# Optimization experiments

Measured on AMD Instinct MI355X. Metric: run time of the kernel, lower is better.

Reference implementation:

```python
import jax, jax.numpy as jnp
import numpy as np

B, N, C, OUT, E = 2, 512, 256, 256, 18


def setup_inputs() -> dict:
    key = jax.random.key(0)
    ks = jax.random.split(key, 16)
    s = 0.05
    w = lambda k, shape: jax.random.normal(k, shape, jnp.float32) * s
    return dict(
        x=jax.random.normal(ks[0], (B, N, C), jnp.float32),
        adjacency=jax.random.randint(ks[1], (B, N, N), 0, 2, jnp.int32),
        edge_feats=jax.random.normal(ks[2], (B, N, N, E), jnp.float32),
        st_w=w(ks[3], (C, OUT)), st_b=jnp.zeros((OUT,), jnp.float32),
        nt_w=w(ks[4], (C, OUT)), nt_b=jnp.zeros((OUT,), jnp.float32),
        em_w1=w(ks[5], (E, 64)), em_b1=jnp.zeros((64,), jnp.float32),
        em_w2=w(ks[6], (64, 64)), em_b2=jnp.zeros((64,), jnp.float32),
        em_w3=w(ks[7], (64, 32)), em_b3=jnp.zeros((32,), jnp.float32),
        at_w1=w(ks[8], (2 * C + 32, 64)), at_b1=jnp.zeros((64,), jnp.float32),
        at_w2=w(ks[9], (64, 32)), at_b2=jnp.zeros((32,), jnp.float32),
        at_w3=w(ks[10], (32, 1)), at_b3=jnp.zeros((1,), jnp.float32),
        eg_w1=w(ks[11], (C + 32, 64)), eg_b1=jnp.zeros((64,), jnp.float32),
        eg_w2=w(ks[12], (64, OUT)), eg_b2=jnp.zeros((OUT,), jnp.float32),
        cb_w1=w(ks[13], (2 * OUT, OUT)), cb_b1=jnp.zeros((OUT,), jnp.float32),
        cb_w2=w(ks[14], (OUT, OUT)), cb_b2=jnp.zeros((OUT,), jnp.float32),
    )


def reference(x, adjacency, edge_feats,
              st_w, st_b, nt_w, nt_b,
              em_w1, em_b1, em_w2, em_b2, em_w3, em_b3,
              at_w1, at_b1, at_w2, at_b2, at_w3, at_b3,
              eg_w1, eg_b1, eg_w2, eg_b2,
              cb_w1, cb_b1, cb_w2, cb_b2):
    c = x.shape[-1]
    mask = adjacency > 0                      # [B,N,N] neighbor mask (j axis = neighbors of i)
    maskf = mask.astype(x.dtype)
    self_feat = x @ st_w + st_b               # [B,N,OUT]
    nbr = x @ nt_w + nt_b                     # [B,N,OUT] transformed neighbor feats
    # edge MLP 18->64->64->32
    pe = jax.nn.relu(edge_feats @ em_w1 + em_b1)
    pe = jax.nn.relu(pe @ em_w2 + em_b2)
    pe = jax.nn.relu(pe @ em_w3 + em_b3)      # [B,N,N,32]
    # attention MLP on concat(x_i, x_j, pe): split first layer to avoid [B,N,N,2C+32]
    a_i = x @ at_w1[:c]                       # [B,N,64]
    a_j = x @ at_w1[c:2 * c]                  # [B,N,64]
    a_e = pe @ at_w1[2 * c:]                  # [B,N,N,64]
    h = jax.nn.relu(a_i[:, :, None, :] + a_j[:, None, :, :] + a_e + at_b1)
    h = jax.nn.relu(h @ at_w2 + at_b2)        # [B,N,N,32]
    scores = (h @ at_w3)[..., 0] + at_b3[0]   # [B,N,N]
    scores = jnp.where(mask, scores, jnp.asarray(-1e9, x.dtype))
    attn = jax.nn.softmax(scores, axis=-1) * maskf  # softmax over neighbor set of each i
    # edge gate on concat(x_j, pe): split first layer
    g = jax.nn.relu((x @ eg_w1[:c])[:, None, :, :] + pe @ eg_w1[c:] + eg_b1)
    g = jax.nn.sigmoid(g @ eg_w2 + eg_b2)     # [B,N,N,OUT]
    gated = g * nbr[:, None, :, :]            # [B,N,N,OUT]
    msg = jnp.einsum('bij,bijc->bic', attn, gated)
    has_nbr = mask.any(axis=-1)[..., None].astype(x.dtype)
    msg = msg * has_nbr                        # nodes with no neighbors get zero message
    comb = jnp.concatenate([self_feat, msg], axis=-1)
    out = jax.nn.relu(comb @ cb_w1 + cb_b1) @ cb_w2 + cb_b2
    return out
```

## Files before the change

### kernel.cpp

```cpp
#include <hip/hip_runtime.h>

#define BB 2
#define NN 512
#define CC 256
#define OO 256
#define EE 18

#define OFF_SF   0
#define OFF_NBR  (BB*NN*OO)
#define OFF_AI   (OFF_NBR + BB*NN*OO)
#define OFF_AJ   (OFF_AI + BB*NN*64)
#define OFF_EGX  (OFF_AJ + BB*NN*64)
#define OFF_MSG  (OFF_EGX + BB*NN*64)
#define OFF_WN   OFF_MSG
#define OFF_W1   OFF_AI
#define OFF_W2   OFF_AJ

typedef float f32x4 __attribute__((ext_vector_type(4)));
typedef __bf16 bf16x8 __attribute__((ext_vector_type(8)));

__device__ __forceinline__ unsigned short f2bf(float f) {
  unsigned u = __float_as_uint(f);
  u += 0x7fffu + ((u >> 16) & 1u);
  return (unsigned short)(u >> 16);
}
__device__ __forceinline__ unsigned pk2(float a, float b) {
  return (unsigned)f2bf(a) | ((unsigned)f2bf(b) << 16);
}
__device__ __forceinline__ unsigned cvtpk(float a, float b) {
  unsigned r;
  asm("v_cvt_pk_bf16_f32 %0, %1, %2" : "=v"(r) : "v"(a), "v"(b));
  return r;
}
__device__ __forceinline__ int swzc(int chunk, int row) {
  return (chunk & ~7) | ((chunk ^ row) & 7);
}

__device__ __forceinline__ f32x4 mfma_bf16(uint4 a, uint4 b, f32x4 c) {
  return __builtin_amdgcn_mfma_f32_16x16x32_bf16(
      __builtin_bit_cast(bf16x8, a), __builtin_bit_cast(bf16x8, b), c, 0, 0, 0);
}

__global__ __launch_bounds__(256) void k_prep_w(
    const float* __restrict__ em_w1, const float* __restrict__ em_w2,
    const float* __restrict__ em_w3, const float* __restrict__ at_w1,
    const float* __restrict__ at_w2, const float* __restrict__ eg_w1,
    const float* __restrict__ eg_w2,
    const float* __restrict__ st_w,  const float* __restrict__ nt_w,
    unsigned char* __restrict__ img, float* __restrict__ ws)
{
  int bid = blockIdx.x;
  if (bid < 120) {
    int idx = bid * 256 + threadIdx.x;
    const float* src; int KV, RO, k, l, ldw;
    if (idx < 2048)       { src = em_w1;          KV = 18; RO = 0;     k = idx>>6;  l = idx&63;  ldw = 64; }
    else if (idx < 6144)  { src = em_w2;          KV = 64; RO = 8192;  int e = idx-2048;  k = e>>6; l = e&63;  ldw = 64; }
    else if (idx < 8192)  { src = em_w3;          KV = 64; RO = 16384; int e = idx-6144;  k = e>>5; l = e&31;  ldw = 32; }
    else if (idx < 10240) { src = at_w1 + 512*64; KV = 32; RO = 20480; int e = idx-8192;  k = e>>6; l = e&63;  ldw = 64; }
    else if (idx < 12288) { src = at_w2;          KV = 64; RO = 28672; int e = idx-10240; k = e>>5; l = e&31;  ldw = 32; }
    else if (idx < 14336) { src = eg_w1 + 256*64; KV = 32; RO = 32768; int e = idx-12288; k = e>>6; l = e&63;  ldw = 64; }
    else                  { src = eg_w2;          KV = 64; RO = 40960; int e = idx-14336; k = e>>8; l = e&255; ldw = 256; }
    float v = (k < KV) ? src[(size_t)k*ldw + l] : 0.f;
    *(unsigned short*)(img + RO + l*128 + ((((k>>3) ^ (l&7))) << 4) + ((k&7) << 1)) = f2bf(v);
  } else {
    unsigned char* dst = (unsigned char*)(ws + OFF_WN);
    int idx = (bid - 120) * 256 + threadIdx.x;
    int col = idx >> 5, ch = idx & 31;
    const float* src; int ld, c;
    if (col < 256)      { src = st_w;           ld = 256; c = col; }
    else if (col < 512) { src = nt_w;           ld = 256; c = col - 256; }
    else if (col < 576) { src = at_w1;          ld = 64;  c = col - 512; }
    else if (col < 640) { src = at_w1 + 256*64; ld = 64;  c = col - 576; }
    else                { src = eg_w1;          ld = 64;  c = col - 640; }
    float e[8];
    #pragma unroll
    for (int q = 0; q < 8; ++q) e[q] = src[(size_t)(ch*8+q)*ld + c];
    uint4 v = make_uint4(pk2(e[0],e[1]), pk2(e[2],e[3]), pk2(e[4],e[5]), pk2(e[6],e[7]));
    *(uint4*)(dst + (size_t)col*512 + swzc(ch, col)*16) = v;
  }
}

__global__ __launch_bounds__(256) void k_prep_out(
    const float* __restrict__ cb_w1, const float* __restrict__ cb_w2,
    float* __restrict__ ws)
{
  int bid = blockIdx.x;
  if (bid < 64) {
    unsigned char* dst = (unsigned char*)(ws + OFF_W1);
    int idx = bid * 256 + threadIdx.x;
    int col = idx >> 6, ch = idx & 63;
    float e[8];
    #pragma unroll
    for (int q = 0; q < 8; ++q) e[q] = cb_w1[(size_t)(ch*8+q)*256 + col];
    uint4 v = make_uint4(pk2(e[0],e[1]), pk2(e[2],e[3]), pk2(e[4],e[5]), pk2(e[6],e[7]));
    *(uint4*)(dst + (size_t)col*1024 + swzc(ch, col)*16) = v;
  } else {
    unsigned char* dst = (unsigned char*)(ws + OFF_W2);
    int idx = (bid - 64) * 256 + threadIdx.x;
    int col = idx >> 5, ch = idx & 31;
    float e[8];
    #pragma unroll
    for (int q = 0; q < 8; ++q) e[q] = cb_w2[(size_t)(ch*8+q)*256 + col];
    uint4 v = make_uint4(pk2(e[0],e[1]), pk2(e[2],e[3]), pk2(e[4],e[5]), pk2(e[6],e[7]));
    *(uint4*)(dst + (size_t)col*512 + swzc(ch, col)*16) = v;
  }
}

__global__ __launch_bounds__(256) void k_node(
    const float* __restrict__ x,
    const float* __restrict__ st_b, const float* __restrict__ nt_b,
    float* __restrict__ ws)
{
  __shared__ __align__(16) unsigned char sA[64*512];
  const int t = threadIdx.x;
  const int c0 = blockIdx.x * 64, g0 = blockIdx.y * 64;

  for (int idx = t; idx < 64*64; idx += 256) {
    int row = idx >> 6, kq = idx & 63;
    float4 v = *(const float4*)(x + (size_t)(g0 + row)*CC + kq*4);
    uint2 p; p.x = pk2(v.x, v.y); p.y = pk2(v.z, v.w);
    *(uint2*)(sA + row*512 + swzc(kq >> 1, row)*16 + (kq & 1)*8) = p;
  }
  __syncthreads();

  const int wid = t >> 6, lane = t & 63, l4 = lane >> 4, l16 = lane & 15;
  const unsigned char* WN = (const unsigned char*)(ws + OFF_WN);

  uint4 af[8];
  {
    int row = wid*16 + l16;
    #pragma unroll
    for (int f = 0; f < 8; ++f)
      af[f] = *(const uint4*)(sA + row*512 + swzc(l4 + 4*f, row)*16);
  }

  const int grow = g0 + wid*16 + l16;
  const int bb = grow >> 9, n0 = grow & 511;

  #pragma unroll
  for (int ct = 0; ct < 4; ++ct) {
    int gcolL = c0 + ct*16 + l16;
    f32x4 acc = {0.f, 0.f, 0.f, 0.f};
    #pragma unroll
    for (int f = 0; f < 8; ++f) {
      uint4 wfr = *(const uint4*)(WN + (size_t)gcolL*512 + swzc(l4 + 4*f, gcolL)*16);
      acc = mfma_bf16(wfr, af[f], acc);
    }
    int gcol0 = c0 + ct*16 + l4*4;
    if (gcol0 < 256) {
      f32x4 bz = *(const f32x4*)(st_b + gcol0);
      f32x4 v = acc + bz;
      *(f32x4*)(ws + OFF_SF + (size_t)grow*OO + gcol0) = v;
    } else if (gcol0 < 512) {
      int c = gcol0 - 256;
      f32x4 bz = *(const f32x4*)(nt_b + c);
      #pragma unroll
      for (int r = 0; r < 4; ++r)
        ws[OFF_NBR + ((size_t)bb*256 + c + r)*512 + n0] = acc[r] + bz[r];
    } else if (gcol0 < 576) {
      *(f32x4*)(ws + OFF_AI + (size_t)grow*64 + (gcol0-512)) = acc;
    } else if (gcol0 < 640) {
      *(f32x4*)(ws + OFF_AJ + (size_t)grow*64 + (gcol0-576)) = acc;
    } else {
      *(f32x4*)(ws + OFF_EGX + (size_t)grow*64 + (gcol0-640)) = acc;
    }
  }
}

__global__ __launch_bounds__(512, 2) void k_edge(
    const int*   __restrict__ adj,
    const float* __restrict__ ef_g,
    const unsigned char* __restrict__ wimg,
    const float* __restrict__ em_b1g, const float* __restrict__ em_b2g,
    const float* __restrict__ em_b3g,
    const float* __restrict__ at_b1g, const float* __restrict__ at_b2g,
    const float* __restrict__ at_w3g, const float* __restrict__ at_b3g,
    const float* __restrict__ eg_b1g, const float* __restrict__ eg_b2g,
    float* __restrict__ ws)
{
  __shared__ __align__(16) unsigned char s_act[512*128];
  __shared__ __align__(16) float s_bem1[64], s_bem2[64], s_bem3[32];
  __shared__ __align__(16) float s_t1init[64], s_bat2[32], s_w3[32];
  __shared__ __align__(16) float s_beg1[64], s_beg2[256];
  __shared__ __align__(16) float s_sc[512];
  __shared__ float s_red[8];
  __shared__ float s_msg[8][256];

  const int t = threadIdx.x;
  const int i = blockIdx.x, b = blockIdx.y;
  const int wid = t >> 6, lane = t & 63, l4 = lane >> 4, l16 = lane & 15;
  const int R = wid * 64;

  const unsigned char* Wem1 = wimg;
  const unsigned char* Wem2 = wimg + 8192;
  const unsigned char* Wem3 = wimg + 16384;
  const unsigned char* Wat1 = wimg + 20480;
  const unsigned char* Wat2 = wimg + 28672;
  const unsigned char* Weg1 = wimg + 32768;
  const unsigned char* Weg2 = wimg + 40960;

  if (t < 64) {
    s_bem1[t]   = em_b1g[t];
    s_bem2[t]   = em_b2g[t];
    s_t1init[t] = ws[OFF_AI + (size_t)(b*NN + i)*64 + t] + at_b1g[t];
    s_beg1[t]   = eg_b1g[t];
  } else if (t < 96)  { s_bem3[t-64]  = em_b3g[t-64]; }
  else if (t < 128)   { s_bat2[t-96]  = at_b2g[t-96]; }
  else if (t < 160)   { s_w3[t-128]   = at_w3g[t-128]; }
  if (t < 256) s_beg2[t] = eg_b2g[t];
  const float atb3 = at_b3g[0];

  const float maskf = adj[(size_t)(b*NN + i)*NN + t] > 0 ? 1.f : 0.f;

  {
    const int j = t;
    const float* efp = ef_g + ((size_t)(b*NN + i)*NN + j) * EE;
    float e[32];
    #pragma unroll
    for (int k = 0; k < 9; ++k) { float2 v2 = *(const float2*)(efp + 2*k); e[2*k] = v2.x; e[2*k+1] = v2.y; }
    #pragma unroll
    for (int k = EE; k < 32; ++k) e[k] = 0.f;
    #pragma unroll
    for (int c = 0; c < 4; ++c) {
      uint4 u = make_uint4(pk2(e[c*8+0],e[c*8+1]), pk2(e[c*8+2],e[c*8+3]),
                           pk2(e[c*8+4],e[c*8+5]), pk2(e[c*8+6],e[c*8+7]));
      *(uint4*)(s_act + j*128 + ((c ^ (j & 7)) << 4)) = u;
    }
  }
  __syncthreads();

  auto loadA = [&](int rb, int f) -> uint4 {
    int rw = rb + l16;
    return *(const uint4*)(s_act + rw*128 + (((l4 + 4*f) ^ (rw & 7)) << 4));
  };
  auto loadB = [&](const unsigned char* w, int ct, int f) -> uint4 {
    int rw = ct*16 + l16;
    return *(const uint4*)(w + rw*128 + (((l4 + 4*f) ^ (rw & 7)) << 4));
  };
  auto storeCT = [&](int rb, int ct, const f32x4& c) {
    int rw = rb + l16;
    int col0 = ct*16 + l4*4;
    uint2 v;
    v.x = cvtpk(fmaxf(c[0], 0.f), fmaxf(c[1], 0.f));
    v.y = cvtpk(fmaxf(c[2], 0.f), fmaxf(c[3], 0.f));
    *(uint2*)(s_act + rw*128 + swzc(col0 >> 3, rw)*16 + (col0 & 7)*2) = v;
  };

  const float* ajR  = ws + OFF_AJ  + (size_t)b*NN*64;
  const float* egR  = ws + OFF_EGX + (size_t)b*NN*64;
  const float* nbrT = ws + OFF_NBR + (size_t)b*256*512;

  uint4 peA[4];

  {
    uint4 W[4];
    #pragma unroll
    for (int ct = 0; ct < 4; ++ct) W[ct] = loadB(Wem1, ct, 0);
    #pragma unroll
    for (int st = 0; st < 4; ++st) {
      int rb = R + st*16;
      uint4 a = loadA(rb, 0);
      #pragma unroll
      for (int ct = 0; ct < 4; ++ct) {
        f32x4 c = *(const f32x4*)&s_bem1[ct*16 + l4*4];
        c = mfma_bf16(W[ct], a, c);
        storeCT(rb, ct, c);
      }
    }
  }
  {
    uint4 W[4][2];
    #pragma unroll
    for (int ct = 0; ct < 4; ++ct) { W[ct][0] = loadB(Wem2, ct, 0); W[ct][1] = loadB(Wem2, ct, 1); }
    #pragma unroll
    for (int st = 0; st < 4; ++st) {
      int rb = R + st*16;
      uint4 a0 = loadA(rb, 0), a1 = loadA(rb, 1);
      #pragma unroll
      for (int ct = 0; ct < 4; ++ct) {
        f32x4 c = *(const f32x4*)&s_bem2[ct*16 + l4*4];
        c = mfma_bf16(W[ct][0], a0, c);
        c = mfma_bf16(W[ct][1], a1, c);
        storeCT(rb, ct, c);
      }
    }
  }
  {
    uint4 W[2][2];
    #pragma unroll
    for (int ct = 0; ct < 2; ++ct) { W[ct][0] = loadB(Wem3, ct, 0); W[ct][1] = loadB(Wem3, ct, 1); }
    #pragma unroll
    for (int st = 0; st < 4; ++st) {
      int rb = R + st*16;
      uint4 a0 = loadA(rb, 0), a1 = loadA(rb, 1);
      #pragma unroll
      for (int ct = 0; ct < 2; ++ct) {
        f32x4 c = *(const f32x4*)&s_bem3[ct*16 + l4*4];
        c = mfma_bf16(W[ct][0], a0, c);
        c = mfma_bf16(W[ct][1], a1, c);
        storeCT(rb, ct, c);
      }
      peA[st] = loadA(rb, 0);
    }
  }
  {
    uint4 W[4];
    #pragma unroll
    for (int ct = 0; ct < 4; ++ct) W[ct] = loadB(Wat1, ct, 0);
    #pragma unroll
    for (int st = 0; st < 4; ++st) {
      int rb = R + st*16;
      int j = rb + l16;
      #pragma unroll
      for (int ct = 0; ct < 4; ++ct) {
        int col0 = ct*16 + l4*4;
        f32x4 ti = *(const f32x4*)&s_t1init[col0];
        f32x4 av = *(const f32x4*)(ajR + (size_t)j*64 + col0);
        f32x4 c = ti + av;
        c = mfma_bf16(W[ct], peA[st], c);
        storeCT(rb, ct, c);
      }
    }
  }
  {
    uint4 W[2][2];
    #pragma unroll
    for (int ct = 0; ct < 2; ++ct) { W[ct][0] = loadB(Wat2, ct, 0); W[ct][1] = loadB(Wat2, ct, 1); }
    #pragma unroll
    for (int st = 0; st < 4; ++st) {
      int rb = R + st*16;
      uint4 a0 = loadA(rb, 0), a1 = loadA(rb, 1);
      f32x4 c0 = *(const f32x4*)&s_bat2[l4*4];
      f32x4 c1 = *(const f32x4*)&s_bat2[16 + l4*4];
      c0 = mfma_bf16(W[0][0], a0, c0); c0 = mfma_bf16(W[0][1], a1, c0);
      c1 = mfma_bf16(W[1][0], a0, c1); c1 = mfma_bf16(W[1][1], a1, c1);
      float val = 0.f;
      #pragma unroll
      for (int r = 0; r < 4; ++r) {
        val += fmaxf(c0[r], 0.f)*s_w3[l4*4 + r];
        val += fmaxf(c1[r], 0.f)*s_w3[16 + l4*4 + r];
      }
      val += __shfl_xor(val, 16);
      val += __shfl_xor(val, 32);
      if (l4 == 0) s_sc[rb + l16] = val + atb3;
    }
  }
  {
    uint4 W[4];
    #pragma unroll
    for (int ct = 0; ct < 4; ++ct) W[ct] = loadB(Weg1, ct, 0);
    #pragma unroll
    for (int st = 0; st < 4; ++st) {
      int rb = R + st*16;
      int j = rb + l16;
      #pragma unroll
      for (int ct = 0; ct < 4; ++ct) {
        int col0 = ct*16 + l4*4;
        f32x4 bg = *(const f32x4*)&s_beg1[col0];
        f32x4 ev = *(const f32x4*)(egR + (size_t)j*64 + col0);
        f32x4 c = bg + ev;
        c = mfma_bf16(W[ct], peA[st], c);
        storeCT(rb, ct, c);
      }
    }
  }
  __syncthreads();

  {
    float v  = maskf > 0.f ? s_sc[t] : -1e9f;
    float m = v;
    #pragma unroll
    for (int d = 1; d < 64; d <<= 1) m = fmaxf(m, __shfl_xor(m, d));
    if (lane == 0) s_red[wid] = m;
    __syncthreads();
    float mx = s_red[0];
    #pragma unroll
    for (int w = 1; w < 8; ++w) mx = fmaxf(mx, s_red[w]);
    float p = maskf > 0.f ? __expf(v - mx) : 0.f;
    float sm = p;
    #pragma unroll
    for (int d = 1; d < 64; d <<= 1) sm += __shfl_xor(sm, d);
    __syncthreads();
    if (lane == 0) s_red[wid] = sm;
    __syncthreads();
    float den = 0.f;
    #pragma unroll
    for (int w = 0; w < 8; ++w) den += s_red[w];
    float inv = den > 0.f ? 1.f/den : 0.f;
    s_sc[t] = p * inv;
  }
  __syncthreads();

  {
    uint4 gA[4][2];
    #pragma unroll
    for (int st = 0; st < 4; ++st) { gA[st][0] = loadA(R + st*16, 0); gA[st][1] = loadA(R + st*16, 1); }

    for (int ct = 0; ct < 16; ++ct) {
      uint4 B0 = loadB(Weg2, ct, 0), B1 = loadB(Weg2, ct, 1);
      int col = ct*16 + l16;
      float bz = s_beg2[col];
      const float* nbrc = nbrT + (size_t)col*512 + R + l4*4;
      float msgp = 0.f;
      #pragma unroll
      for (int st = 0; st < 4; ++st) {
        f32x4 nv = *(const f32x4*)(nbrc + st*16);
        f32x4 at = *(const f32x4*)(&s_sc[R + st*16 + l4*4]);
        f32x4 c = {bz, bz, bz, bz};
        c = mfma_bf16(gA[st][0], B0, c);
        c = mfma_bf16(gA[st][1], B1, c);
        #pragma unroll
        for (int r = 0; r < 4; ++r) {
          float g = __builtin_amdgcn_rcpf(1.f + __expf(-c[r]));
          msgp += g * at[r] * nv[r];
        }
      }
      msgp += __shfl_xor(msgp, 16);
      msgp += __shfl_xor(msgp, 32);
      if (lane < 16) s_msg[wid][ct*16 + lane] = msgp;
    }
  }
  __syncthreads();
  if (t < 256) {
    float s = 0.f;
    #pragma unroll
    for (int w = 0; w < 8; ++w) s += s_msg[w][t];
    ws[OFF_MSG + (size_t)(b*NN + i)*OO + t] = s;
  }
}

__global__ __launch_bounds__(256) void k_out(
    const float* __restrict__ cb_b1, const float* __restrict__ cb_b2,
    const float* __restrict__ ws, float* __restrict__ out)
{
  __shared__ __align__(16) unsigned char sA[16*1024];
  __shared__ __align__(16) unsigned char sT[16*512];
  const int t = threadIdx.x;
  const int g0 = blockIdx.x * 16;

  for (int idx = t; idx < 16*128; idx += 256) {
    int row = idx >> 7, kq = idx & 127;
    const float* src = (kq < 64)
        ? ws + OFF_SF  + (size_t)(g0 + row)*OO + kq*4
        : ws + OFF_MSG + (size_t)(g0 + row)*OO + (kq - 64)*4;
    float4 v = *(const float4*)src;
    uint2 p; p.x = pk2(v.x, v.y); p.y = pk2(v.z, v.w);
    *(uint2*)(sA + row*1024 + swzc(kq >> 1, row)*16 + (kq & 1)*8) = p;
  }
  __syncthreads();

  const int wid = t >> 6, lane = t & 63, l4 = lane >> 4, l16 = lane & 15;
  const unsigned char* W1 = (const unsigned char*)(ws + OFF_W1);
  const unsigned char* W2 = (const unsigned char*)(ws + OFF_W2);

  {
    uint4 af[16];
    #pragma unroll
    for (int f = 0; f < 16; ++f)
      af[f] = *(const uint4*)(sA + l16*1024 + swzc(l4 + 4*f, l16)*16);
    #pragma unroll
    for (int c = 0; c < 4; ++c) {
      int col = wid*64 + c*16 + l16;
      float bz = cb_b1[col];
      f32x4 acc = {bz, bz, bz, bz};
      #pragma unroll
      for (int f = 0; f < 16; ++f) {
        uint4 bfr = *(const uint4*)(W1 + (size_t)col*1024 + swzc(l4 + 4*f, col)*16);
        acc = mfma_bf16(af[f], bfr, acc);
      }
      #pragma unroll
      for (int r = 0; r < 4; ++r) {
        int row = l4*4 + r;
        *(unsigned short*)(sT + row*512 + swzc(col >> 3, row)*16 + (col & 7)*2)
            = f2bf(fmaxf(acc[r], 0.f));
      }
    }
  }
  __syncthreads();

  {
    uint4 tf[8];
    #pragma unroll
    for (int f = 0; f < 8; ++f)
      tf[f] = *(const uint4*)(sT + l16*512 + swzc(l4 + 4*f, l16)*16);
    #pragma unroll
    for (int c = 0; c < 4; ++c) {
      int col = wid*64 + c*16 + l16;
      float bz = cb_b2[col];
      f32x4 acc = {bz, bz, bz, bz};
      #pragma unroll
      for (int f = 0; f < 8; ++f) {
        uint4 bfr = *(const uint4*)(W2 + (size_t)col*512 + swzc(l4 + 4*f, col)*16);
        acc = mfma_bf16(tf[f], bfr, acc);
      }
      #pragma unroll
      for (int r = 0; r < 4; ++r)
        out[(size_t)(g0 + l4*4 + r)*OO + col] = acc[r];
    }
  }
}

extern "C" void kernel_launch(void* const* d_in, const int* in_sizes, int n_in,
                              void* d_out, int out_size, void* d_ws, size_t ws_size,
                              hipStream_t stream) {
  const float* x     = (const float*)d_in[0];
  const int*   adj   = (const int*)  d_in[1];
  const float* ef    = (const float*)d_in[2];
  const float* st_w  = (const float*)d_in[3];
  const float* st_b  = (const float*)d_in[4];
  const float* nt_w  = (const float*)d_in[5];
  const float* nt_b  = (const float*)d_in[6];
  const float* em_w1 = (const float*)d_in[7];
  const float* em_b1 = (const float*)d_in[8];
  const float* em_w2 = (const float*)d_in[9];
  const float* em_b2 = (const float*)d_in[10];
  const float* em_w3 = (const float*)d_in[11];
  const float* em_b3 = (const float*)d_in[12];
  const float* at_w1 = (const float*)d_in[13];
  const float* at_b1 = (const float*)d_in[14];
  const float* at_w2 = (const float*)d_in[15];
  const float* at_b2 = (const float*)d_in[16];
  const float* at_w3 = (const float*)d_in[17];
  const float* at_b3 = (const float*)d_in[18];
  const float* eg_w1 = (const float*)d_in[19];
  const float* eg_b1 = (const float*)d_in[20];
  const float* eg_w2 = (const float*)d_in[21];
  const float* eg_b2 = (const float*)d_in[22];
  const float* cb_w1 = (const float*)d_in[23];
  const float* cb_b1 = (const float*)d_in[24];
  const float* cb_w2 = (const float*)d_in[25];
  const float* cb_b2 = (const float*)d_in[26];
  float* ws  = (float*)d_ws;
  float* out = (float*)d_out;
  unsigned char* wimg = (unsigned char*)d_out;

  k_prep_w<<<dim3(208), dim3(256), 0, stream>>>(em_w1, em_w2, em_w3, at_w1, at_w2,
      eg_w1, eg_w2, st_w, nt_w, wimg, ws);
  k_node<<<dim3(11, 16), dim3(256), 0, stream>>>(x, st_b, nt_b, ws);
  k_edge<<<dim3(NN, BB), dim3(512), 0, stream>>>(adj, ef, wimg,
      em_b1, em_b2, em_b3, at_b1, at_b2, at_w3, at_b3, eg_b1, eg_b2, ws);
  k_prep_out<<<dim3(96), dim3(256), 0, stream>>>(cb_w1, cb_w2, ws);
  k_out<<<dim3(64), dim3(256), 0, stream>>>(cb_b1, cb_b2, ws, out);
}
```

Measured before the change: 141.0 us.

## Process neighbors in two half-passes to halve LDS and defer softmax normalization

The edge kernel now handles the 512 neighbors in two passes of 256, which halves the shared activation buffer and the score buffer. The goal is to fit more blocks per CU and to remove the block-wide max/sum softmax barriers. Softmax no longer subtracts the max: it accumulates exp(score) directly and divides the final message by the summed denominator, so large scores could overflow. Edge-feature loading is also split across lane pairs.

```diff
diff --git a/kernel.cpp b/kernel.cpp
--- a/kernel.cpp
+++ b/kernel.cpp
@@ -178,18 +178,18 @@
     const float* __restrict__ eg_b1g, const float* __restrict__ eg_b2g,
     float* __restrict__ ws)
 {
-  __shared__ __align__(16) unsigned char s_act[512*128];
+  __shared__ __align__(16) unsigned char s_act[256*128];
   __shared__ __align__(16) float s_bem1[64], s_bem2[64], s_bem3[32];
   __shared__ __align__(16) float s_t1init[64], s_bat2[32], s_w3[32];
   __shared__ __align__(16) float s_beg1[64], s_beg2[256];
-  __shared__ __align__(16) float s_sc[512];
+  __shared__ __align__(16) float s_sc[256];
+  __shared__ __align__(16) float s_msg[8][256];
   __shared__ float s_red[8];
-  __shared__ float s_msg[8][256];
 
   const int t = threadIdx.x;
   const int i = blockIdx.x, b = blockIdx.y;
   const int wid = t >> 6, lane = t & 63, l4 = lane >> 4, l16 = lane & 15;
-  const int R = wid * 64;
+  const int SB = wid * 32;
 
   const unsigned char* Wem1 = wimg;
   const unsigned char* Wem2 = wimg + 8192;
@@ -209,24 +209,6 @@
   else if (t < 160)   { s_w3[t-128]   = at_w3g[t-128]; }
   if (t < 256) s_beg2[t] = eg_b2g[t];
   const float atb3 = at_b3g[0];
-
-  const float maskf = adj[(size_t)(b*NN + i)*NN + t] > 0 ? 1.f : 0.f;
-
-  {
-    const int j = t;
-    const float* efp = ef_g + ((size_t)(b*NN + i)*NN + j) * EE;
-    float e[32];
-    #pragma unroll
-    for (int k = 0; k < 9; ++k) { float2 v2 = *(const float2*)(efp + 2*k); e[2*k] = v2.x; e[2*k+1] = v2.y; }
-    #pragma unroll
-    for (int k = EE; k < 32; ++k) e[k] = 0.f;
-    #pragma unroll
-    for (int c = 0; c < 4; ++c) {
-      uint4 u = make_uint4(pk2(e[c*8+0],e[c*8+1]), pk2(e[c*8+2],e[c*8+3]),
-                           pk2(e[c*8+4],e[c*8+5]), pk2(e[c*8+6],e[c*8+7]));
-      *(uint4*)(s_act + j*128 + ((c ^ (j & 7)) << 4)) = u;
-    }
-  }
   __syncthreads();
 
   auto loadA = [&](int rb, int f) -> uint4 {
@@ -249,183 +231,202 @@
   const float* ajR  = ws + OFF_AJ  + (size_t)b*NN*64;
   const float* egR  = ws + OFF_EGX + (size_t)b*NN*64;
   const float* nbrT = ws + OFF_NBR + (size_t)b*256*512;
-
-  uint4 peA[4];
-
-  {
-    uint4 W[4];
-    #pragma unroll
-    for (int ct = 0; ct < 4; ++ct) W[ct] = loadB(Wem1, ct, 0);
-    #pragma unroll
-    for (int st = 0; st < 4; ++st) {
-      int rb = R + st*16;
-      uint4 a = loadA(rb, 0);
-      #pragma unroll
-      for (int ct = 0; ct < 4; ++ct) {
-        f32x4 c = *(const f32x4*)&s_bem1[ct*16 + l4*4];
-        c = mfma_bf16(W[ct], a, c);
-        storeCT(rb, ct, c);
-      }
-    }
-  }
-  {
-    uint4 W[4][2];
-    #pragma unroll
-    for (int ct = 0; ct < 4; ++ct) { W[ct][0] = loadB(Wem2, ct, 0); W[ct][1] = loadB(Wem2, ct, 1); }
-    #pragma unroll
-    for (int st = 0; st < 4; ++st) {
-      int rb = R + st*16;
-      uint4 a0 = loadA(rb, 0), a1 = loadA(rb, 1);
-      #pragma unroll
-      for (int ct = 0; ct < 4; ++ct) {
-        f32x4 c = *(const f32x4*)&s_bem2[ct*16 + l4*4];
-        c = mfma_bf16(W[ct][0], a0, c);
-        c = mfma_bf16(W[ct][1], a1, c);
-        storeCT(rb, ct, c);
-      }
-    }
-  }
-  {
-    uint4 W[2][2];
-    #pragma unroll
-    for (int ct = 0; ct < 2; ++ct) { W[ct][0] = loadB(Wem3, ct, 0); W[ct][1] = loadB(Wem3, ct, 1); }
-    #pragma unroll
-    for (int st = 0; st < 4; ++st) {
-      int rb = R + st*16;
-      uint4 a0 = loadA(rb, 0), a1 = loadA(rb, 1);
-      #pragma unroll
-      for (int ct = 0; ct < 2; ++ct) {
-        f32x4 c = *(const f32x4*)&s_bem3[ct*16 + l4*4];
-        c = mfma_bf16(W[ct][0], a0, c);
-        c = mfma_bf16(W[ct][1], a1, c);
-        storeCT(rb, ct, c);
-      }
-      peA[st] = loadA(rb, 0);
-    }
-  }
-  {
-    uint4 W[4];
-    #pragma unroll
-    for (int ct = 0; ct < 4; ++ct) W[ct] = loadB(Wat1, ct, 0);
-    #pragma unroll
-    for (int st = 0; st < 4; ++st) {
-      int rb = R + st*16;
-      int j = rb + l16;
-      #pragma unroll
-      for (int ct = 0; ct < 4; ++ct) {
-        int col0 = ct*16 + l4*4;
-        f32x4 ti = *(const f32x4*)&s_t1init[col0];
-        f32x4 av = *(const f32x4*)(ajR + (size_t)j*64 + col0);
-        f32x4 c = ti + av;
-        c = mfma_bf16(W[ct], peA[st], c);
-        storeCT(rb, ct, c);
-      }
-    }
-  }
-  {
-    uint4 W[2][2];
-    #pragma unroll
-    for (int ct = 0; ct < 2; ++ct) { W[ct][0] = loadB(Wat2, ct, 0); W[ct][1] = loadB(Wat2, ct, 1); }
-    #pragma unroll
-    for (int st = 0; st < 4; ++st) {
-      int rb = R + st*16;
-      uint4 a0 = loadA(rb, 0), a1 = loadA(rb, 1);
-      f32x4 c0 = *(const f32x4*)&s_bat2[l4*4];
-      f32x4 c1 = *(const f32x4*)&s_bat2[16 + l4*4];
-      c0 = mfma_bf16(W[0][0], a0, c0); c0 = mfma_bf16(W[0][1], a1, c0);
-      c1 = mfma_bf16(W[1][0], a0, c1); c1 = mfma_bf16(W[1][1], a1, c1);
-      float val = 0.f;
-      #pragma unroll
-      for (int r = 0; r < 4; ++r) {
-        val += fmaxf(c0[r], 0.f)*s_w3[l4*4 + r];
-        val += fmaxf(c1[r], 0.f)*s_w3[16 + l4*4 + r];
-      }
-      val += __shfl_xor(val, 16);
-      val += __shfl_xor(val, 32);
-      if (l4 == 0) s_sc[rb + l16] = val + atb3;
-    }
-  }
-  {
-    uint4 W[4];
-    #pragma unroll
-    for (int ct = 0; ct < 4; ++ct) W[ct] = loadB(Weg1, ct, 0);
-    #pragma unroll
-    for (int st = 0; st < 4; ++st) {
-      int rb = R + st*16;
-      int j = rb + l16;
-      #pragma unroll
-      for (int ct = 0; ct < 4; ++ct) {
-        int col0 = ct*16 + l4*4;
-        f32x4 bg = *(const f32x4*)&s_beg1[col0];
-        f32x4 ev = *(const f32x4*)(egR + (size_t)j*64 + col0);
-        f32x4 c = bg + ev;
-        c = mfma_bf16(W[ct], peA[st], c);
-        storeCT(rb, ct, c);
-      }
-    }
-  }
+  const int*   adjr = adj + (size_t)(b*NN + i)*NN;
+  const float* efrow= ef_g + (size_t)(b*NN + i)*NN*EE;
+
+  float denacc = 0.f;
+
+  #pragma unroll
+  for (int p = 0; p < 2; ++p) {
+    const int jbase = p * 256;
+
+    {
+      int s = SB + (lane >> 1);
+      int cpair = (lane & 1) * 2;
+      const float* efp = efrow + (size_t)(jbase + s) * EE;
+      uint4 u0, u1;
+      if ((lane & 1) == 0) {
+        float e[16];
+        #pragma unroll
+        for (int k = 0; k < 8; ++k) { float2 v2 = *(const float2*)(efp + 2*k); e[2*k] = v2.x; e[2*k+1] = v2.y; }
+        u0 = make_uint4(pk2(e[0],e[1]), pk2(e[2],e[3]), pk2(e[4],e[5]), pk2(e[6],e[7]));
+        u1 = make_uint4(pk2(e[8],e[9]), pk2(e[10],e[11]), pk2(e[12],e[13]), pk2(e[14],e[15]));
+      } else {
+        float2 v2 = *(const float2*)(efp + 16);
+        u0 = make_uint4(pk2(v2.x, v2.y), 0u, 0u, 0u);
+        u1 = make_uint4(0u, 0u, 0u, 0u);
+      }
+      *(uint4*)(s_act + s*128 + ((cpair     ^ (s & 7)) << 4)) = u0;
+      *(uint4*)(s_act + s*128 + (((cpair+1) ^ (s & 7)) << 4)) = u1;
+    }
+
+    uint4 peA[2];
+
+    {
+      uint4 W[4];
+      #pragma unroll
+      for (int ct = 0; ct < 4; ++ct) W[ct] = loadB(Wem1, ct, 0);
+      #pragma unroll
+      for (int st = 0; st < 2; ++st) {
+        int rb = SB + st*16;
+        uint4 a = loadA(rb, 0);
+        #pragma unroll
+        for (int ct = 0; ct < 4; ++ct) {
+          f32x4 c = *(const f32x4*)&s_bem1[ct*16 + l4*4];
+          c = mfma_bf16(W[ct], a, c);
+          storeCT(rb, ct, c);
+        }
+      }
+    }
+    {
+      uint4 W[4][2];
+      #pragma unroll
+      for (int ct = 0; ct < 4; ++ct) { W[ct][0] = loadB(Wem2, ct, 0); W[ct][1] = loadB(Wem2, ct, 1); }
+      #pragma unroll
+      for (int st = 0; st < 2; ++st) {
+        int rb = SB + st*16;
+        uint4 a0 = loadA(rb, 0), a1 = loadA(rb, 1);
+        #pragma unroll
+        for (int ct = 0; ct < 4; ++ct) {
+          f32x4 c = *(const f32x4*)&s_bem2[ct*16 + l4*4];
+          c = mfma_bf16(W[ct][0], a0, c);
+          c = mfma_bf16(W[ct][1], a1, c);
+          storeCT(rb, ct, c);
+        }
+      }
+    }
+    {
+      uint4 W[2][2];
+      #pragma unroll
+      for (int ct = 0; ct < 2; ++ct) { W[ct][0] = loadB(Wem3, ct, 0); W[ct][1] = loadB(Wem3, ct, 1); }
+      #pragma unroll
+      for (int st = 0; st < 2; ++st) {
+        int rb = SB + st*16;
+        uint4 a0 = loadA(rb, 0), a1 = loadA(rb, 1);
+        #pragma unroll
+        for (int ct = 0; ct < 2; ++ct) {
+          f32x4 c = *(const f32x4*)&s_bem3[ct*16 + l4*4];
+          c = mfma_bf16(W[ct][0], a0, c);
+          c = mfma_bf16(W[ct][1], a1, c);
+          storeCT(rb, ct, c);
+        }
+        peA[st] = loadA(rb, 0);
+      }
+    }
+    {
+      uint4 W[4];
+      #pragma unroll
+      for (int ct = 0; ct < 4; ++ct) W[ct] = loadB(Wat1, ct, 0);
+      #pragma unroll
+      for (int st = 0; st < 2; ++st) {
+        int rb = SB + st*16;
+        int jg = jbase + rb + l16;
+        #pragma unroll
+        for (int ct = 0; ct < 4; ++ct) {
+          int col0 = ct*16 + l4*4;
+          f32x4 ti = *(const f32x4*)&s_t1init[col0];
+          f32x4 av = *(const f32x4*)(ajR + (size_t)jg*64 + col0);
+          f32x4 c = ti + av;
+          c = mfma_bf16(W[ct], peA[st], c);
+          storeCT(rb, ct, c);
+        }
+      }
+    }
+    {
+      uint4 W[2][2];
+      #pragma unroll
+      for (int ct = 0; ct < 2; ++ct) { W[ct][0] = loadB(Wat2, ct, 0); W[ct][1] = loadB(Wat2, ct, 1); }
+      #pragma unroll
+      for (int st = 0; st < 2; ++st) {
+        int rb = SB + st*16;
+        uint4 a0 = loadA(rb, 0), a1 = loadA(rb, 1);
+        f32x4 c0 = *(const f32x4*)&s_bat2[l4*4];
+        f32x4 c1 = *(const f32x4*)&s_bat2[16 + l4*4];
+        c0 = mfma_bf16(W[0][0], a0, c0); c0 = mfma_bf16(W[0][1], a1, c0);
+        c1 = mfma_bf16(W[1][0], a0, c1); c1 = mfma_bf16(W[1][1], a1, c1);
+        float val = 0.f;
+        #pragma unroll
+        for (int r = 0; r < 4; ++r) {
+          val += fmaxf(c0[r], 0.f)*s_w3[l4*4 + r];
+          val += fmaxf(c1[r], 0.f)*s_w3[16 + l4*4 + r];
+        }
+        val += __shfl_xor(val, 16);
+        val += __shfl_xor(val, 32);
+        if (l4 == 0) {
+          int jg = jbase + rb + l16;
+          float pj = (adjr[jg] > 0) ? __expf(val + atb3) : 0.f;
+          s_sc[rb + l16] = pj;
+          denacc += pj;
+        }
+      }
+    }
+    {
+      uint4 W[4];
+      #pragma unroll
+      for (int ct = 0; ct < 4; ++ct) W[ct] = loadB(Weg1, ct, 0);
+      #pragma unroll
+      for (int st = 0; st < 2; ++st) {
+        int rb = SB + st*16;
+        int jg = jbase + rb + l16;
+        #pragma unroll
+        for (int ct = 0; ct < 4; ++ct) {
+          int col0 = ct*16 + l4*4;
+          f32x4 bg = *(const f32x4*)&s_beg1[col0];
+          f32x4 ev = *(const f32x4*)(egR + (size_t)jg*64 + col0);
+          f32x4 c = bg + ev;
+          c = mfma_bf16(W[ct], peA[st], c);
+          storeCT(rb, ct, c);
+        }
+      }
+    }
+    {
+      uint4 gA[2][2];
+      #pragma unroll
+      for (int st = 0; st < 2; ++st) { gA[st][0] = loadA(SB + st*16, 0); gA[st][1] = loadA(SB + st*16, 1); }
+
+      for (int ct = 0; ct < 16; ++ct) {
+        uint4 B0 = loadB(Weg2, ct, 0), B1 = loadB(Weg2, ct, 1);
+        int col = ct*16 + l16;
+        float bz = s_beg2[col];
+        float mp = 0.f;
+        #pragma unroll
+        for (int st = 0; st < 2; ++st) {
+          int rb = SB + st*16;
+          f32x4 nv = *(const f32x4*)(nbrT + (size_t)col*512 + jbase + rb + l4*4);
+          f32x4 at = *(const f32x4*)(&s_sc[rb + l4*4]);
+          f32x4 c = {bz, bz, bz, bz};
+          c = mfma_bf16(gA[st][0], B0, c);
+          c = mfma_bf16(gA[st][1], B1, c);
+          #pragma unroll
+          for (int r = 0; r < 4; ++r) {
+            float g = __builtin_amdgcn_rcpf(1.f + __expf(-c[r]));
+            mp += g * at[r] * nv[r];
+          }
+        }
+        mp += __shfl_xor(mp, 16);
+        mp += __shfl_xor(mp, 32);
+        if (lane < 16) {
+          if (p == 0) s_msg[wid][ct*16 + lane] = mp;
+          else        s_msg[wid][ct*16 + lane] += mp;
+        }
+      }
+    }
+  }
+
+  denacc += __shfl_xor(denacc, 1);  denacc += __shfl_xor(denacc, 2);
+  denacc += __shfl_xor(denacc, 4);  denacc += __shfl_xor(denacc, 8);
+  denacc += __shfl_xor(denacc, 16); denacc += __shfl_xor(denacc, 32);
+  if (lane == 0) s_red[wid] = denacc;
   __syncthreads();
-
-  {
-    float v  = maskf > 0.f ? s_sc[t] : -1e9f;
-    float m = v;
-    #pragma unroll
-    for (int d = 1; d < 64; d <<= 1) m = fmaxf(m, __shfl_xor(m, d));
-    if (lane == 0) s_red[wid] = m;
-    __syncthreads();
-    float mx = s_red[0];
-    #pragma unroll
-    for (int w = 1; w < 8; ++w) mx = fmaxf(mx, s_red[w]);
-    float p = maskf > 0.f ? __expf(v - mx) : 0.f;
-    float sm = p;
-    #pragma unroll
-    for (int d = 1; d < 64; d <<= 1) sm += __shfl_xor(sm, d);
-    __syncthreads();
-    if (lane == 0) s_red[wid] = sm;
-    __syncthreads();
+  if (t < 256) {
     float den = 0.f;
     #pragma unroll
     for (int w = 0; w < 8; ++w) den += s_red[w];
     float inv = den > 0.f ? 1.f/den : 0.f;
-    s_sc[t] = p * inv;
-  }
-  __syncthreads();
-
-  {
-    uint4 gA[4][2];
-    #pragma unroll
-    for (int st = 0; st < 4; ++st) { gA[st][0] = loadA(R + st*16, 0); gA[st][1] = loadA(R + st*16, 1); }
-
-    for (int ct = 0; ct < 16; ++ct) {
-      uint4 B0 = loadB(Weg2, ct, 0), B1 = loadB(Weg2, ct, 1);
-      int col = ct*16 + l16;
-      float bz = s_beg2[col];
-      const float* nbrc = nbrT + (size_t)col*512 + R + l4*4;
-      float msgp = 0.f;
-      #pragma unroll
-      for (int st = 0; st < 4; ++st) {
-        f32x4 nv = *(const f32x4*)(nbrc + st*16);
-        f32x4 at = *(const f32x4*)(&s_sc[R + st*16 + l4*4]);
-        f32x4 c = {bz, bz, bz, bz};
-        c = mfma_bf16(gA[st][0], B0, c);
-        c = mfma_bf16(gA[st][1], B1, c);
-        #pragma unroll
-        for (int r = 0; r < 4; ++r) {
-          float g = __builtin_amdgcn_rcpf(1.f + __expf(-c[r]));
-          msgp += g * at[r] * nv[r];
-        }
-      }
-      msgp += __shfl_xor(msgp, 16);
-      msgp += __shfl_xor(msgp, 32);
-      if (lane < 16) s_msg[wid][ct*16 + lane] = msgp;
-    }
-  }
-  __syncthreads();
-  if (t < 256) {
     float s = 0.f;
     #pragma unroll
     for (int w = 0; w < 8; ++w) s += s_msg[w][t];
-    ws[OFF_MSG + (size_t)(b*NN + i)*OO + t] = s;
+    ws[OFF_MSG + (size_t)(b*NN + i)*OO + t] = s * inv;
   }
 }
 
```

New measurement: 167.8 us (median of 2 runs). 1.19x slower.
